# Performance work log

Measured on AMD Instinct MI355X. Metric: run time of the kernel, lower is better.

Reference implementation:

```python
import jax, jax.numpy as jnp
import numpy as np

B, S, D, H = 16, 1024, 512, 8
DH = D // H


def setup_inputs() -> dict:
    key = jax.random.key(0)
    ks = jax.random.split(key, 8)
    q = jax.random.normal(ks[0], (B, S, D), dtype=jnp.float32)
    k = jax.random.normal(ks[1], (B, S, D), dtype=jnp.float32)
    v = jax.random.normal(ks[2], (B, S, D), dtype=jnp.float32)
    # causal lower-triangular mask (1 = attend), broadcastable [1,1,S,S]
    mask = jnp.tril(jnp.ones((S, S), dtype=jnp.int32))[None, None]
    # xavier-uniform weights, zero biases (matches _reset_parameters)
    def xavier(rk, fan):
        lim = float(np.sqrt(6.0 / (fan + fan)))
        return jax.random.uniform(rk, (fan, fan), jnp.float32, -lim, lim)
    Wk = xavier(ks[3], D)
    Wv = xavier(ks[4], D)
    Wo = xavier(ks[5], D)
    bk = jnp.zeros((D,), jnp.float32)
    bv = jnp.zeros((D,), jnp.float32)
    bo = jnp.zeros((D,), jnp.float32)
    return {"q": q, "k": k, "v": v, "mask": mask,
            "Wk": Wk, "bk": bk, "Wv": Wv, "bv": bv, "Wo": Wo, "bo": bo,
            "zero_pad": 1}


def reference(q, k, v, mask, Wk, bk, Wv, bv, Wo, bo, zero_pad):
    # key_query_same=True: q and k both use key_linear
    def split_heads(x):  # [B,S,D] -> [B,H,S,DH]
        return x.reshape(B, S, H, DH).transpose(0, 2, 1, 3)

    qh = split_heads(q @ Wk.T + bk)
    kh = split_heads(k @ Wk.T + bk)
    vh = split_heads(v @ Wv.T + bv)

    scores = jnp.einsum('bhqd,bhkd->bhqk', qh, kh) / jnp.sqrt(jnp.float32(DH))
    scores = jnp.where(mask == 0, jnp.float32(-1e32), scores)
    attn = jax.nn.softmax(scores, axis=-1)
    if zero_pad:  # zero out attention of the first query position (simpleKT trick)
        attn = attn.at[:, :, 0, :].set(0.0)
    # dropout p=0.0 (eval) -> identity
    out = jnp.einsum('bhqk,bhkd->bhqd', attn, vh)  # [B,H,S,DH]
    concat = out.transpose(0, 2, 1, 3).reshape(B, S, D)
    return concat @ Wo.T + bo
```

## Files before the change

kernel.cpp:

```cpp
#include <hip/hip_runtime.h>
#include <hip/hip_bf16.h>
#include <math.h>


typedef __attribute__((ext_vector_type(4))) float f32x4;
typedef __attribute__((ext_vector_type(8))) short bf16x8;

__device__ __forceinline__ short f2bf(float f) {
    union { float f; unsigned u; } x; x.f = f;
    unsigned r = x.u + 0x7fffu + ((x.u >> 16) & 1u);
    return (short)(r >> 16);
}
__device__ __forceinline__ short bfscale(short s, float f) {
    union { float f; unsigned u; } x; x.u = ((unsigned)(unsigned short)s) << 16;
    return f2bf(x.f * f);
}

__device__ __forceinline__ void gload_lds16(const void* g, void* l) {
    __builtin_amdgcn_global_load_lds(
        (const __attribute__((address_space(1))) unsigned int*)g,
        (__attribute__((address_space(3))) unsigned int*)l, 16, 0, 0);
}

__global__ void cvt_w_kernel(const float* __restrict__ w0, const float* __restrict__ w1,
                             const float* __restrict__ w2,
                             short* __restrict__ o0, short* __restrict__ o1,
                             short* __restrict__ o2)
{
    int z = blockIdx.y;
    const float* src = z == 0 ? w0 : (z == 1 ? w1 : w2);
    short* dst = z == 0 ? o0 : (z == 1 ? o1 : o2);
    int i = (blockIdx.x * 256 + threadIdx.x) * 4;
    float4 f = *(const float4*)(src + i);
    short4 s;
    s.x = f2bf(f.x); s.y = f2bf(f.y); s.z = f2bf(f.z); s.w = f2bf(f.w);
    *(short4*)(dst + i) = s;
}

template<int IN_BF16, int SPLIT>
__device__ __forceinline__ void gemm_body(const void* __restrict__ Xv,
                                          const short* __restrict__ W,
                                          const float* __restrict__ bias,
                                          void* __restrict__ Out,
                                          int m0, int n0)
{
    constexpr int ASTR = IN_BF16 ? 64 : 72;
    __shared__ short As[128 * ASTR];
    __shared__ short Bs[128 * 64];
    int tid = threadIdx.x;
    int lane = tid & 63, w = tid >> 6;
    int wr = (w >> 1) * 64, wc = (w & 1) * 64;
    int fr = lane & 15, hi = lane >> 4;
    int lrow = lane >> 3;
    int gcol = ((lane & 7) ^ (lrow & 3)) * 8;
    int xsw = ((hi ^ (lane & 3)) * 8);
    f32x4 acc[4][4] = {};

    const float* Xf = (const float*)Xv;
    const short* Xb = (const short*)Xv;

    float4 pf[8];
    if (!IN_BF16) {
        #pragma unroll
        for (int p = 0; p < 8; ++p) {
            int e = (p * 256 + tid) * 4;
            pf[p] = *(const float4*)(Xf + (size_t)(m0 + (e >> 6)) * 512 + (e & 63));
        }
    }

    for (int k0 = 0; k0 < 512; k0 += 64) {
        __syncthreads();
        #pragma unroll
        for (int c = 0; c < 4; ++c) {
            int chunk = w * 4 + c;
            gload_lds16(W + (size_t)(n0 + chunk * 8 + lrow) * 512 + k0 + gcol,
                        &Bs[chunk * 512]);
        }
        if (IN_BF16) {
            #pragma unroll
            for (int c = 0; c < 4; ++c) {
                int chunk = w * 4 + c;
                gload_lds16(Xb + (size_t)(m0 + chunk * 8 + lrow) * 512 + k0 + gcol,
                            &As[chunk * 512]);
            }
        } else {
            #pragma unroll
            for (int p = 0; p < 8; ++p) {
                int e = (p * 256 + tid) * 4;
                short4 s;
                s.x = f2bf(pf[p].x); s.y = f2bf(pf[p].y);
                s.z = f2bf(pf[p].z); s.w = f2bf(pf[p].w);
                *(short4*)&As[(e >> 6) * ASTR + (e & 63)] = s;
            }
        }
        __syncthreads();
        if (!IN_BF16 && k0 + 64 < 512) {
            #pragma unroll
            for (int p = 0; p < 8; ++p) {
                int e = (p * 256 + tid) * 4;
                pf[p] = *(const float4*)(Xf + (size_t)(m0 + (e >> 6)) * 512 + k0 + 64 + (e & 63));
            }
        }
        #pragma unroll
        for (int ks = 0; ks < 2; ++ks) {
            bf16x8 a[4], b[4];
            #pragma unroll
            for (int i = 0; i < 4; ++i) {
                int row = wr + i * 16 + fr;
                a[i] = IN_BF16
                    ? *(const bf16x8*)&As[row * ASTR + ks * 32 + xsw]
                    : *(const bf16x8*)&As[row * ASTR + ks * 32 + hi * 8];
            }
            #pragma unroll
            for (int j = 0; j < 4; ++j)
                b[j] = *(const bf16x8*)&Bs[(wc + j * 16 + fr) * 64 + ks * 32 + xsw];
            #pragma unroll
            for (int i = 0; i < 4; ++i)
                #pragma unroll
                for (int j = 0; j < 4; ++j)
                    acc[i][j] = __builtin_amdgcn_mfma_f32_16x16x32_bf16(a[i], b[j], acc[i][j], 0, 0, 0);
        }
    }
    int row4 = (lane >> 4) * 4;
    #pragma unroll
    for (int i = 0; i < 4; ++i) {
        #pragma unroll
        for (int j = 0; j < 4; ++j) {
            int gn = n0 + wc + j * 16 + fr;
            float bb = bias[gn];
            #pragma unroll
            for (int r = 0; r < 4; ++r) {
                int gm = m0 + wr + i * 16 + row4 + r;
                float v = acc[i][j][r] + bb;
                if (SPLIT == 1) {
                    int bidx = gm >> 10, s = gm & 1023, hh = gn >> 6, dh = gn & 63;
                    ((short*)Out)[((((size_t)bidx * 8 + hh) * 1024) + s) * 64 + dh] = f2bf(v);
                } else if (SPLIT == 2) {
                    int bidx = gm >> 10, s = gm & 1023, hh = gn >> 6, dh = gn & 63;
                    ((short*)Out)[((((size_t)bidx * 8 + hh) * 64) + dh) * 1024 + s] = f2bf(v);
                } else {
                    ((float*)Out)[(size_t)gm * 512 + gn] = v;
                }
            }
        }
    }
}

__global__ __launch_bounds__(256, 3) void proj_qk_kernel(
    const float* __restrict__ q, const float* __restrict__ k,
    const short* __restrict__ wk, const float* __restrict__ bk,
    short* __restrict__ qh, short* __restrict__ kh)
{
    int d = blockIdx.x;
    int wg = (d & 7) * 128 + (d >> 3);
    int z = wg >> 9;
    int rem = wg & 511;
    gemm_body<0, 1>(z ? (const void*)k : (const void*)q, wk, bk,
                    z ? (void*)kh : (void*)qh,
                    (rem >> 2) * 128, (rem & 3) * 128);
}

__global__ __launch_bounds__(256, 3) void proj_v_kernel(
    const float* __restrict__ v, const short* __restrict__ wv,
    const float* __restrict__ bv, short* __restrict__ vh)
{
    int d = blockIdx.x;
    int wg = (d & 7) * 64 + (d >> 3);
    gemm_body<0, 2>(v, wv, bv, vh, (wg >> 2) * 128, (wg & 3) * 128);
}

__global__ __launch_bounds__(256, 3) void proj_o_kernel(
    const short* __restrict__ ob, const short* __restrict__ wo,
    const float* __restrict__ bo, float* __restrict__ out)
{
    int d = blockIdx.x;
    int wg = (d & 7) * 64 + (d >> 3);
    gemm_body<1, 0>(ob, wo, bo, out, (wg >> 2) * 128, (wg & 3) * 128);
}

__global__ __launch_bounds__(256, 3) void attn_kernel(
    const short* __restrict__ QH, const short* __restrict__ KH,
    const short* __restrict__ VT, short* __restrict__ O,
    const int* __restrict__ zp)
{
    __shared__ short Ks[2][64][68];
    __shared__ short Vt[2][64][68];
    __shared__ short Ps[4][16][76];
    int tid = threadIdx.x, lane = tid & 63, w = tid >> 6;
    int fr = lane & 15, hi = lane >> 4;
    int d = blockIdx.x;
    int bh = (d & 7) * 16 + ((d >> 3) & 15);
    int qtp = d >> 7;
    const size_t basebh = (size_t)bh << 16;
    const short* Kb = KH + basebh;
    const short* Vb = VT + basebh;
    int r0 = tid >> 3, c0 = (tid & 7) * 8;
    int zero = zp[0];
    int b = bh >> 3, h = bh & 7;
    const float csc = 0.125f * 1.44269504f;

    for (int which = 0; which < 2; ++which) {
        int qt = which ? 15 - qtp : qtp;
        int qrow0 = qt * 64 + w * 16;

        bf16x8 aQ[2];
        {
            const short* qp = QH + basebh + (size_t)(qrow0 + fr) * 64 + hi * 8;
            bf16x8 q0 = *(const bf16x8*)qp;
            bf16x8 q1 = *(const bf16x8*)(qp + 32);
            #pragma unroll
            for (int j = 0; j < 8; ++j) {
                aQ[0][j] = bfscale(q0[j], csc);
                aQ[1][j] = bfscale(q1[j], csc);
            }
        }

        f32x4 oacc[4] = {};
        float lsum[4] = {0.f, 0.f, 0.f, 0.f};

        bf16x8 kA, kB, vA, vB;
        kA = *(const bf16x8*)(Kb + r0 * 64 + c0);
        kB = *(const bf16x8*)(Kb + (r0 + 32) * 64 + c0);
        vA = *(const bf16x8*)(Vb + (size_t)r0 * 1024 + c0);
        vB = *(const bf16x8*)(Vb + (size_t)(r0 + 32) * 1024 + c0);
        *(bf16x8*)&Ks[0][r0][c0] = kA;
        *(bf16x8*)&Ks[0][r0 + 32][c0] = kB;
        *(bf16x8*)&Vt[0][r0][c0] = vA;
        *(bf16x8*)&Vt[0][r0 + 32][c0] = vB;
        if (qt > 0) {
            const short* kp = Kb + 4096;
            const short* vp = Vb + 64;
            kA = *(const bf16x8*)(kp + r0 * 64 + c0);
            kB = *(const bf16x8*)(kp + (r0 + 32) * 64 + c0);
            vA = *(const bf16x8*)(vp + (size_t)r0 * 1024 + c0);
            vB = *(const bf16x8*)(vp + (size_t)(r0 + 32) * 1024 + c0);
        }
        __syncthreads();

        for (int kt = 0; kt <= qt; ++kt) {
            int cur = kt & 1;
            if (kt < qt) {
                *(bf16x8*)&Ks[cur ^ 1][r0][c0] = kA;
                *(bf16x8*)&Ks[cur ^ 1][r0 + 32][c0] = kB;
                *(bf16x8*)&Vt[cur ^ 1][r0][c0] = vA;
                *(bf16x8*)&Vt[cur ^ 1][r0 + 32][c0] = vB;
                if (kt + 1 < qt) {
                    const short* kp = Kb + (kt + 2) * 4096;
                    const short* vp = Vb + (kt + 2) * 64;
                    kA = *(const bf16x8*)(kp + r0 * 64 + c0);
                    kB = *(const bf16x8*)(kp + (r0 + 32) * 64 + c0);
                    vA = *(const bf16x8*)(vp + (size_t)r0 * 1024 + c0);
                    vB = *(const bf16x8*)(vp + (size_t)(r0 + 32) * 1024 + c0);
                }
            }

            f32x4 sa[4] = {};
            #pragma unroll
            for (int kf = 0; kf < 4; ++kf)
                #pragma unroll
                for (int ks = 0; ks < 2; ++ks) {
                    bf16x8 kb = *(const bf16x8*)&Ks[cur][kf * 16 + fr][ks * 32 + hi * 8];
                    sa[kf] = __builtin_amdgcn_mfma_f32_16x16x32_bf16(aQ[ks], kb, sa[kf], 0, 0, 0);
                }

            if (kt == qt) {
                #pragma unroll
                for (int kf = 0; kf < 4; ++kf) {
                    int gk = kt * 64 + kf * 16 + fr;
                    #pragma unroll
                    for (int r = 0; r < 4; ++r) {
                        float p = exp2f(sa[kf][r]);
                        if (gk > qrow0 + hi * 4 + r) p = 0.f;
                        lsum[r] += p;
                        union { float f; unsigned u; } c; c.f = p;
                        Ps[w][hi * 4 + r][kf * 16 + fr] = (short)(c.u >> 16);
                    }
                }
            } else {
                #pragma unroll
                for (int kf = 0; kf < 4; ++kf)
                    #pragma unroll
                    for (int r = 0; r < 4; ++r) {
                        float p = exp2f(sa[kf][r]);
                        lsum[r] += p;
                        union { float f; unsigned u; } c; c.f = p;
                        Ps[w][hi * 4 + r][kf * 16 + fr] = (short)(c.u >> 16);
                    }
            }

            bf16x8 pa[2];
            pa[0] = *(const bf16x8*)&Ps[w][fr][hi * 8];
            pa[1] = *(const bf16x8*)&Ps[w][fr][32 + hi * 8];
            #pragma unroll
            for (int df = 0; df < 4; ++df)
                #pragma unroll
                for (int ks = 0; ks < 2; ++ks) {
                    bf16x8 vb = *(const bf16x8*)&Vt[cur][df * 16 + fr][ks * 32 + hi * 8];
                    oacc[df] = __builtin_amdgcn_mfma_f32_16x16x32_bf16(pa[ks], vb, oacc[df], 0, 0, 0);
                }
            __syncthreads();
        }

        float inv[4];
        #pragma unroll
        for (int r = 0; r < 4; ++r) {
            float rs = lsum[r];
            #pragma unroll
            for (int off = 1; off < 16; off <<= 1) rs += __shfl_xor(rs, off);
            inv[r] = 1.0f / rs;
        }
        #pragma unroll
        for (int df = 0; df < 4; ++df)
            #pragma unroll
            for (int r = 0; r < 4; ++r) {
                int gq = qrow0 + hi * 4 + r;
                float v = oacc[df][r] * inv[r];
                if (zero && gq == 0) v = 0.f;
                O[((size_t)(b * 1024 + gq)) * 512 + h * 64 + df * 16 + fr] = f2bf(v);
            }
    }
}

extern "C" void kernel_launch(void* const* d_in, const int* in_sizes, int n_in,
                              void* d_out, int out_size, void* d_ws, size_t ws_size,
                              hipStream_t stream)
{
    const float* q  = (const float*)d_in[0];
    const float* k  = (const float*)d_in[1];
    const float* v  = (const float*)d_in[2];
    const float* Wk = (const float*)d_in[4];
    const float* bk = (const float*)d_in[5];
    const float* Wv = (const float*)d_in[6];
    const float* bv = (const float*)d_in[7];
    const float* Wo = (const float*)d_in[8];
    const float* bo = (const float*)d_in[9];
    const int*   zp = (const int*)d_in[10];
    float* out = (float*)d_out;

    short* wkb = (short*)d_ws;
    short* wvb = wkb + 262144;
    short* wob = wvb + 262144;
    short* qh  = wob + 262144;
    short* kh  = qh + 8388608;
    short* vh  = kh + 8388608;
    short* ob  = vh + 8388608;

    cvt_w_kernel<<<dim3(256, 3, 1), 256, 0, stream>>>(Wk, Wv, Wo, wkb, wvb, wob);
    proj_qk_kernel<<<dim3(1024, 1, 1), 256, 0, stream>>>(q, k, wkb, bk, qh, kh);
    proj_v_kernel<<<dim3(512, 1, 1), 256, 0, stream>>>(v, wvb, bv, vh);
    attn_kernel<<<dim3(1024, 1, 1), 256, 0, stream>>>(qh, kh, vh, ob, zp);
    proj_o_kernel<<<dim3(512, 1, 1), 256, 0, stream>>>(ob, wob, bo, out);
}
```

Measured before the change: 118.8 us.

## Keep attention probabilities in registers via transposed QK MFMA and lane shuffles

The QK^T MFMA operands are swapped so each lane holds scores for one query row across several keys. The probabilities are then packed to bf16 pairs and redistributed into the PV A-operand layout with cross-lane shuffles instead of a round trip through the per-wave LDS P buffer. This also shrinks the row-sum reduction to two xor shuffles, and dropping the LDS buffer lets launch bounds rise to 4 blocks per CU. The cost is 16 ds_bpermute shuffles per tile, plus extra selects and higher register pressure under the tighter occupancy bound.

```diff
diff --git a/kernel.cpp b/kernel.cpp
--- a/kernel.cpp
+++ b/kernel.cpp
@@ -14,6 +14,10 @@
 __device__ __forceinline__ short bfscale(short s, float f) {
     union { float f; unsigned u; } x; x.u = ((unsigned)(unsigned short)s) << 16;
     return f2bf(x.f * f);
+}
+__device__ __forceinline__ unsigned packbf(float a, float b) {
+    union { float f; unsigned u; } xa, xb; xa.f = a; xb.f = b;
+    return (xa.u >> 16) | (xb.u & 0xffff0000u);
 }
 
 __device__ __forceinline__ void gload_lds16(const void* g, void* l) {
@@ -178,14 +182,13 @@
     gemm_body<1, 0>(ob, wo, bo, out, (wg >> 2) * 128, (wg & 3) * 128);
 }
 
-__global__ __launch_bounds__(256, 3) void attn_kernel(
+__global__ __launch_bounds__(256, 4) void attn_kernel(
     const short* __restrict__ QH, const short* __restrict__ KH,
     const short* __restrict__ VT, short* __restrict__ O,
     const int* __restrict__ zp)
 {
     __shared__ short Ks[2][64][68];
     __shared__ short Vt[2][64][68];
-    __shared__ short Ps[4][16][76];
     int tid = threadIdx.x, lane = tid & 63, w = tid >> 6;
     int fr = lane & 15, hi = lane >> 4;
     int d = blockIdx.x;
@@ -198,6 +201,9 @@
     int zero = zp[0];
     int b = bh >> 3, h = bh & 7;
     const float csc = 0.125f * 1.44269504f;
+    int srcA = fr + 16 * ((2 * hi) & 3);
+    int srcB = fr + 16 * ((2 * hi + 1) & 3);
+    bool hi2 = hi >= 2;
 
     for (int which = 0; which < 2; ++which) {
         int qt = which ? 15 - qtp : qtp;
@@ -216,7 +222,7 @@
         }
 
         f32x4 oacc[4] = {};
-        float lsum[4] = {0.f, 0.f, 0.f, 0.f};
+        float lsum = 0.f;
 
         bf16x8 kA, kB, vA, vB;
         kA = *(const bf16x8*)(Kb + r0 * 64 + c0);
@@ -260,37 +266,57 @@
                 #pragma unroll
                 for (int ks = 0; ks < 2; ++ks) {
                     bf16x8 kb = *(const bf16x8*)&Ks[cur][kf * 16 + fr][ks * 32 + hi * 8];
-                    sa[kf] = __builtin_amdgcn_mfma_f32_16x16x32_bf16(aQ[ks], kb, sa[kf], 0, 0, 0);
-                }
-
+                    sa[kf] = __builtin_amdgcn_mfma_f32_16x16x32_bf16(kb, aQ[ks], sa[kf], 0, 0, 0);
+                }
+
+            unsigned pk[4][2];
             if (kt == qt) {
+                int gq = fr + w * 16;
                 #pragma unroll
                 for (int kf = 0; kf < 4; ++kf) {
-                    int gk = kt * 64 + kf * 16 + fr;
+                    float t[4];
                     #pragma unroll
                     for (int r = 0; r < 4; ++r) {
+                        int gk = kf * 16 + hi * 4 + r;
                         float p = exp2f(sa[kf][r]);
-                        if (gk > qrow0 + hi * 4 + r) p = 0.f;
-                        lsum[r] += p;
-                        union { float f; unsigned u; } c; c.f = p;
-                        Ps[w][hi * 4 + r][kf * 16 + fr] = (short)(c.u >> 16);
+                        if (gk > gq) p = 0.f;
+                        t[r] = p;
                     }
+                    lsum += (t[0] + t[1]) + (t[2] + t[3]);
+                    pk[kf][0] = packbf(t[0], t[1]);
+                    pk[kf][1] = packbf(t[2], t[3]);
                 }
             } else {
                 #pragma unroll
-                for (int kf = 0; kf < 4; ++kf)
+                for (int kf = 0; kf < 4; ++kf) {
+                    float t[4];
                     #pragma unroll
-                    for (int r = 0; r < 4; ++r) {
-                        float p = exp2f(sa[kf][r]);
-                        lsum[r] += p;
-                        union { float f; unsigned u; } c; c.f = p;
-                        Ps[w][hi * 4 + r][kf * 16 + fr] = (short)(c.u >> 16);
-                    }
+                    for (int r = 0; r < 4; ++r) t[r] = exp2f(sa[kf][r]);
+                    lsum += (t[0] + t[1]) + (t[2] + t[3]);
+                    pk[kf][0] = packbf(t[0], t[1]);
+                    pk[kf][1] = packbf(t[2], t[3]);
+                }
             }
 
             bf16x8 pa[2];
-            pa[0] = *(const bf16x8*)&Ps[w][fr][hi * 8];
-            pa[1] = *(const bf16x8*)&Ps[w][fr][32 + hi * 8];
+            #pragma unroll
+            for (int ks = 0; ks < 2; ++ks) {
+                unsigned a0 = __shfl((int)pk[2 * ks][0], srcA);
+                unsigned a1 = __shfl((int)pk[2 * ks][1], srcA);
+                unsigned b0 = __shfl((int)pk[2 * ks + 1][0], srcA);
+                unsigned b1 = __shfl((int)pk[2 * ks + 1][1], srcA);
+                unsigned c0w = __shfl((int)pk[2 * ks][0], srcB);
+                unsigned c1 = __shfl((int)pk[2 * ks][1], srcB);
+                unsigned d0 = __shfl((int)pk[2 * ks + 1][0], srcB);
+                unsigned d1 = __shfl((int)pk[2 * ks + 1][1], srcB);
+                union { unsigned u[4]; bf16x8 v; } pu;
+                pu.u[0] = hi2 ? b0 : a0;
+                pu.u[1] = hi2 ? b1 : a1;
+                pu.u[2] = hi2 ? d0 : c0w;
+                pu.u[3] = hi2 ? d1 : c1;
+                pa[ks] = pu.v;
+            }
+
             #pragma unroll
             for (int df = 0; df < 4; ++df)
                 #pragma unroll
@@ -301,20 +327,19 @@
             __syncthreads();
         }
 
-        float inv[4];
-        #pragma unroll
-        for (int r = 0; r < 4; ++r) {
-            float rs = lsum[r];
-            #pragma unroll
-            for (int off = 1; off < 16; off <<= 1) rs += __shfl_xor(rs, off);
-            inv[r] = 1.0f / rs;
-        }
+        float rs = lsum;
+        rs += __shfl_xor(rs, 16);
+        rs += __shfl_xor(rs, 32);
+        float inv = 1.0f / rs;
+        float invr[4];
+        #pragma unroll
+        for (int r = 0; r < 4; ++r) invr[r] = __shfl(inv, hi * 4 + r);
         #pragma unroll
         for (int df = 0; df < 4; ++df)
             #pragma unroll
             for (int r = 0; r < 4; ++r) {
                 int gq = qrow0 + hi * 4 + r;
-                float v = oacc[df][r] * inv[r];
+                float v = oacc[df][r] * invr[r];
                 if (zero && gq == 0) v = 0.f;
                 O[((size_t)(b * 1024 + gq)) * 512 + h * 64 + df * 16 + fr] = f2bf(v);
             }
```

Result: slower. 122.1 us (+2.9%).
